# Optimization experiments

Measured on AMD Instinct MI355X. Metric: run time of the kernel, lower is better.

## Reference

```python
import jax, jax.numpy as jnp
import numpy as np

EMB = 128
EA = 32
ET = 32
N = 50000
E = 500000
EPS = 1e-5
DROP_P = 0.1


def setup_inputs() -> dict:
    key = jax.random.key(0)
    ks = jax.random.split(key, 12)
    din = EMB + EA + ET
    return {
        "hidden": jax.random.normal(ks[0], (N, EMB), jnp.float32),
        "edge_index": jax.random.randint(ks[1], (2, E), 0, N, jnp.int64 if jax.config.jax_enable_x64 else jnp.int32),
        "edge_attr": jax.random.normal(ks[2], (E, EA), jnp.float32),
        "edge_time_emb": jax.random.normal(ks[3], (E, ET), jnp.float32),
        "boundary_condition": jax.random.normal(ks[4], (N, EMB), jnp.float32),
        # learned params (torch Linear stored transposed: [in, out])
        "W_msg": jax.random.normal(ks[5], (din, EMB), jnp.float32) / np.sqrt(din),
        "b_msg": jnp.zeros((EMB,), jnp.float32),
        "W_lin": jax.random.normal(ks[6], (EMB, EMB), jnp.float32) / np.sqrt(EMB),
        "b_lin": jnp.zeros((EMB,), jnp.float32),
        "ln_gamma": jnp.ones((EMB,), jnp.float32),
        "ln_beta": jnp.zeros((EMB,), jnp.float32),
    }


def reference(hidden, edge_index, edge_attr, edge_time_emb, boundary_condition,
              W_msg, b_msg, W_lin, b_lin, ln_gamma, ln_beta):
    num_nodes = hidden.shape[0]
    # gather source node features, concat with edge features -> [E, emb+ea+et]
    msg = jnp.concatenate([hidden[edge_index[0]], edge_attr, edge_time_emb], axis=1)
    msg = jax.nn.relu(msg @ W_msg + b_msg)                      # [E, emb]
    # append boundary condition as self-loop messages
    msg_aug = jnp.concatenate([msg, boundary_condition], axis=0)
    idx_aug = jnp.concatenate([edge_index[1], jnp.arange(num_nodes, dtype=edge_index.dtype)])
    out = jax.ops.segment_sum(msg_aug, idx_aug, num_segments=num_nodes)  # scatter-sum [N, emb]
    out = out @ W_lin + b_lin
    # LayerNorm (eps=1e-5, affine)
    mean = out.mean(-1, keepdims=True)
    var = out.var(-1, keepdims=True)
    out = (out - mean) * jax.lax.rsqrt(var + EPS) * ln_gamma + ln_beta
    out = jax.nn.relu(out)
    # dropout p=0.1, training=True (fixed key for reproducibility)
    keep = jax.random.bernoulli(jax.random.key(42), 1.0 - DROP_P, out.shape)
    out = jnp.where(keep, out / (1.0 - DROP_P), 0.0)
    return out
```

## Files before the change

### kernel.cpp

```cpp
#include <hip/hip_runtime.h>
#include <stdint.h>

#define NN 50000
#define NE 500000
#define NEPAD 500032
#define SPB 64
#define HP_BLOCKS ((NN + 127) / 128)
#define DEG_STRIDE (HP_BLOCKS * 256)
#define NBLK_N ((NN + 255) / 256)

typedef short bf16x8 __attribute__((ext_vector_type(8)));
typedef float f32x4 __attribute__((ext_vector_type(4)));
typedef unsigned short u16;
typedef unsigned short u16x4 __attribute__((ext_vector_type(4)));
typedef unsigned int u32x4 __attribute__((ext_vector_type(4)));

__device__ __forceinline__ u16 f2b(float x) {
  uint32_t u = __builtin_bit_cast(uint32_t, x);
  return (u16)((u + 0x7fffu + ((u >> 16) & 1u)) >> 16);
}
__device__ __forceinline__ float b2f(uint32_t lo16) {
  return __builtin_bit_cast(float, lo16 << 16);
}

__device__ __forceinline__ void threefry(uint32_t x0, uint32_t x1,
                                         uint32_t& o0, uint32_t& o1) {
  const uint32_t k0 = 0u, k1 = 42u, k2 = 0u ^ 42u ^ 0x1BD11BDAu;
  x0 += k0; x1 += k1;
#define TFR(r) { x0 += x1; x1 = (x1 << r) | (x1 >> (32 - r)); x1 ^= x0; }
  TFR(13) TFR(15) TFR(26) TFR(6)
  x0 += k1; x1 += k2 + 1u;
  TFR(17) TFR(29) TFR(16) TFR(24)
  x0 += k2; x1 += k0 + 2u;
  TFR(13) TFR(15) TFR(26) TFR(6)
  x0 += k0; x1 += k1 + 3u;
  TFR(17) TFR(29) TFR(16) TFR(24)
  x0 += k1; x1 += k2 + 4u;
  TFR(13) TFR(15) TFR(26) TFR(6)
  x0 += k2; x1 += k0 + 5u;
#undef TFR
  o0 = x0; o1 = x1;
}

__device__ __forceinline__ bool jax_keep(uint32_t j) {
  uint32_t o0, o1;
  threefry(0u, j, o0, o1);
  uint32_t bits = o0 ^ o1;
  float u = __builtin_bit_cast(float, (bits >> 9) | 0x3f800000u) - 1.0f;
  return u < 0.9f;
}

template <int K, int GM>
__device__ __forceinline__ void mfma_tile(const u16* sA, const u16* sBT,
                                          int t, f32x4 (&c)[4][4]) {
  const int lane = t & 63, w = t >> 6;
  const int wr = (w & 1) << 6, wc = (w >> 1) << 6;
  const int quad = lane >> 4, lr = lane & 15;
#pragma unroll
  for (int i = 0; i < 4; ++i)
#pragma unroll
    for (int j = 0; j < 4; ++j) { f32x4 z = {0.f, 0.f, 0.f, 0.f}; c[i][j] = z; }
#pragma unroll
  for (int ks = 0; ks < K; ks += 32) {
    const int kg = (ks >> 3) + quad;
    bf16x8 a[4], b[4];
#pragma unroll
    for (int i = 0; i < 4; ++i) {
      int row = wr + (i << 4) + lr;
      a[i] = *(const bf16x8*)&sA[row * K + ((kg ^ (row & GM)) << 3)];
    }
#pragma unroll
    for (int j = 0; j < 4; ++j) {
      int row = wc + (j << 4) + lr;
      b[j] = *(const bf16x8*)&sBT[row * K + ((kg ^ (row & GM)) << 3)];
    }
#pragma unroll
    for (int i = 0; i < 4; ++i)
#pragma unroll
      for (int j = 0; j < 4; ++j)
        c[i][j] = __builtin_amdgcn_mfma_f32_16x16x32_bf16(a[i], b[j], c[i][j], 0, 0, 0);
  }
}

__global__ __launch_bounds__(256) void k_scan1(const uint32_t* __restrict__ deg,
                                               uint32_t* __restrict__ ex,
                                               uint32_t* __restrict__ bsum) {
  __shared__ uint32_t s[256];
  int t = threadIdx.x;
  int i = blockIdx.x * 256 + t;
  uint32_t v = (i < NN) ? deg[i] : 0u;
  s[t] = v;
  __syncthreads();
#pragma unroll
  for (int off = 1; off < 256; off <<= 1) {
    uint32_t y = (t >= off) ? s[t - off] : 0u;
    __syncthreads();
    s[t] += y;
    __syncthreads();
  }
  if (i < NN) ex[i] = s[t] - v;
  if (t == 255) bsum[blockIdx.x] = s[255];
}

__global__ __launch_bounds__(256) void k_scan2(const uint32_t* __restrict__ bsum,
                                               uint32_t* __restrict__ boff) {
  __shared__ uint32_t s[256];
  int t = threadIdx.x;
  uint32_t v = (t < NBLK_N) ? bsum[t] : 0u;
  s[t] = v;
  __syncthreads();
#pragma unroll
  for (int off = 1; off < 256; off <<= 1) {
    uint32_t y = (t >= off) ? s[t - off] : 0u;
    __syncthreads();
    s[t] += y;
    __syncthreads();
  }
  boff[t] = s[t] - v;
}

__global__ __launch_bounds__(256) void k_scan3(const uint32_t* __restrict__ ex,
                                               const uint32_t* __restrict__ boff,
                                               uint32_t* __restrict__ cursor) {
  int i = blockIdx.x * 256 + threadIdx.x;
  if (i < NN) cursor[i] = ex[i] + boff[blockIdx.x];
}

__global__ __launch_bounds__(256) void k_perm_s(const int* __restrict__ ei,
                                                const float* __restrict__ attr,
                                                const float* __restrict__ tim,
                                                uint32_t* __restrict__ cursor,
                                                u16* __restrict__ Asorted,
                                                int* __restrict__ srcp,
                                                int* __restrict__ dstp) {
  const int t = threadIdx.x;
  const int j = t & 7;
  const long e = (long)blockIdx.x * 32 + (t >> 3);
  const bool v = e < NE;
  int src = 0, dst = 0;
  uint32_t pos = 0;
  if (v && j == 0) {
    src = ei[e];
    dst = ei[NE + e];
    pos = atomicAdd(&cursor[dst], 1u);
  }
  pos = __shfl(pos, 0, 8);
  src = __shfl(src, 0, 8);
  dst = __shfl(dst, 0, 8);
  if (v) {
    f32x4 va = *(const f32x4*)(attr + ((size_t)e << 5) + (j << 2));
    f32x4 vt = *(const f32x4*)(tim + ((size_t)e << 5) + (j << 2));
    u16x4 ba = {f2b(va[0]), f2b(va[1]), f2b(va[2]), f2b(va[3])};
    u16x4 bt = {f2b(vt[0]), f2b(vt[1]), f2b(vt[2]), f2b(vt[3])};
    *(u16x4*)&Asorted[((size_t)pos << 6) + (j << 2)] = ba;
    *(u16x4*)&Asorted[((size_t)pos << 6) + 32 + (j << 2)] = bt;
    if (j == 0) { srcp[pos] = src; dstp[pos] = dst; }
  }
}

__global__ __launch_bounds__(256) void k_perm_f(const int* __restrict__ ei,
                                                uint32_t* __restrict__ cursor,
                                                int* __restrict__ perm,
                                                int* __restrict__ srcp,
                                                int* __restrict__ dstp) {
  int i = blockIdx.x * 256 + threadIdx.x;
  if (i < NE) {
    int s = ei[i], d = ei[NE + i];
    uint32_t pos = atomicAdd(&cursor[d], 1u);
    perm[pos] = i;
    srcp[pos] = s;
    dstp[pos] = d;
  }
}

__global__ __launch_bounds__(256) void k_hp(const float* __restrict__ hidden,
                                            const float* __restrict__ Wmsg,
                                            const float* __restrict__ bmsg,
                                            const int* __restrict__ ei,
                                            uint32_t* __restrict__ deg,
                                            u16* __restrict__ Hp,
                                            u16* __restrict__ WcImg) {
  __shared__ u16 sA[128 * 128];
  __shared__ u16 sBT[128 * 128];
  const int t = threadIdx.x;
  const int row0 = blockIdx.x << 7;
  for (int i = blockIdx.x * 256 + t; i < NE; i += DEG_STRIDE)
    atomicAdd(&deg[ei[NE + i]], 1u);
  if (blockIdx.x == 0) {
#pragma unroll
    for (int it = 0; it < 32; ++it) {
      int li = t + (it << 8);
      int k = li >> 7, d = li & 127;
      WcImg[(d << 6) + k] = f2b(Wmsg[16384 + li]);
    }
  }
#pragma unroll
  for (int it = 0; it < 16; ++it) {
    int li = t + (it << 8);
    int row = li >> 5, c4 = li & 31;
    int n = row0 + row;
    f32x4 v = {0.f, 0.f, 0.f, 0.f};
    if (n < NN) v = *(const f32x4*)(hidden + ((size_t)n << 7) + (c4 << 2));
    u16x4 b = {f2b(v[0]), f2b(v[1]), f2b(v[2]), f2b(v[3])};
    *(u16x4*)&sA[(row << 7) + ((((c4 >> 1) ^ (row & 15)) << 3) + ((c4 & 1) << 2))] = b;
  }
#pragma unroll
  for (int it = 0; it < 64; ++it) {
    int li = t + (it << 8);
    int k = li >> 7, d = li & 127;
    sBT[(d << 7) + ((((k >> 3) ^ (d & 15)) << 3) + (k & 7))] = f2b(Wmsg[li]);
  }
  __syncthreads();
  f32x4 c[4][4];
  mfma_tile<128, 15>(sA, sBT, t, c);
  const int lane = t & 63, w = t >> 6;
  const int wr = (w & 1) << 6, wc = (w >> 1) << 6;
  const int quad = lane >> 4, lr = lane & 15;
#pragma unroll
  for (int j = 0; j < 4; ++j) {
    int d = wc + (j << 4) + lr;
    float bias = bmsg[d];
#pragma unroll
    for (int i = 0; i < 4; ++i) {
      int nb = row0 + wr + (i << 4) + (quad << 2);
#pragma unroll
      for (int r = 0; r < 4; ++r) {
        int n = nb + r;
        if (n < NN) Hp[((size_t)n << 7) + d] = f2b(c[i][j][r] + bias);
      }
    }
  }
}

template <bool SORTED>
__global__ __launch_bounds__(256, 4) void k_edge3(const float* __restrict__ attr,
                                                  const float* __restrict__ tim,
                                                  const int* __restrict__ perm,
                                                  const u16* __restrict__ Asorted,
                                                  const u16* __restrict__ WcImg,
                                                  const int* __restrict__ srcp,
                                                  const int* __restrict__ dstp,
                                                  const u16* __restrict__ Hp,
                                                  float* __restrict__ acc) {
  __shared__ union { u16 A[64 * 64]; float C[64 * 128]; } lds;
  __shared__ int sdst[64];
  const int t = threadIdx.x;
  const long e0 = (long)blockIdx.x << 6;

  if (!SORTED) {
#pragma unroll
    for (int it = 0; it < 2; ++it) {
      int li = t + (it << 8);
      int row = li >> 3, c4 = li & 7;
      long sg = e0 + row;
      f32x4 va = {0.f, 0.f, 0.f, 0.f}, vt = {0.f, 0.f, 0.f, 0.f};
      if (sg < NE) {
        int e = perm[sg];
        va = *(const f32x4*)(attr + ((size_t)e << 5) + (c4 << 2));
        vt = *(const f32x4*)(tim + ((size_t)e << 5) + (c4 << 2));
      }
      int g0 = c4 >> 1, h = (c4 & 1) << 2;
      u16x4 ba = {f2b(va[0]), f2b(va[1]), f2b(va[2]), f2b(va[3])};
      u16x4 bt = {f2b(vt[0]), f2b(vt[1]), f2b(vt[2]), f2b(vt[3])};
      *(u16x4*)&lds.A[(row << 6) + (((g0 ^ (row & 7)) << 3) + h)] = ba;
      *(u16x4*)&lds.A[(row << 6) + ((((g0 + 4) ^ (row & 7)) << 3) + h)] = bt;
    }
  }
  const int s = t >> 2, q = t & 3;
  const long sg1 = e0 + s;
  const bool v1 = sg1 < NE;
  int src = 0, dstn = -1;
  if (v1) { src = srcp[sg1]; dstn = dstp[sg1]; }
  u32x4 hp[4];
  if (v1) {
    const u32x4* hp4 = (const u32x4*)(Hp + ((size_t)src << 7) + (q << 5));
#pragma unroll
    for (int g = 0; g < 4; ++g) hp[g] = hp4[g];
  }
  if (q == 0) sdst[s] = v1 ? dstn : -1;
  __syncthreads();

  const int lane = t & 63, w = t >> 6;
  const int quad = lane >> 4, lr = lane & 15;
  f32x4 c[4][2];
#pragma unroll
  for (int i = 0; i < 4; ++i)
#pragma unroll
    for (int j = 0; j < 2; ++j) { f32x4 z = {0.f, 0.f, 0.f, 0.f}; c[i][j] = z; }
#pragma unroll
  for (int ks = 0; ks < 64; ks += 32) {
    const int gi = (ks >> 3) + quad;
    bf16x8 a[4], b[2];
#pragma unroll
    for (int i = 0; i < 4; ++i) {
      int row = (i << 4) + lr;
      if (SORTED)
        a[i] = *(const bf16x8*)&Asorted[((size_t)(e0 + row) << 6) + (gi << 3)];
      else
        a[i] = *(const bf16x8*)&lds.A[(row << 6) + ((gi ^ (row & 7)) << 3)];
    }
#pragma unroll
    for (int j = 0; j < 2; ++j) {
      int col = (w << 5) + (j << 4) + lr;
      b[j] = *(const bf16x8*)&WcImg[(col << 6) + (gi << 3)];
    }
#pragma unroll
    for (int i = 0; i < 4; ++i)
#pragma unroll
      for (int j = 0; j < 2; ++j)
        c[i][j] = __builtin_amdgcn_mfma_f32_16x16x32_bf16(a[i], b[j], c[i][j], 0, 0, 0);
  }
  __syncthreads();
#pragma unroll
  for (int i = 0; i < 4; ++i)
#pragma unroll
    for (int j = 0; j < 2; ++j)
#pragma unroll
      for (int r = 0; r < 4; ++r) {
        int row = (i << 4) + (quad << 2) + r;
        int col = (w << 5) + (j << 4) + lr;
        lds.C[(row << 7) + ((((col >> 2) ^ (row & 31)) << 2) + (col & 3))] = c[i][j][r];
      }
  __syncthreads();
  if (v1) {
#pragma unroll
    for (int g = 0; g < 8; ++g) {
      int cb = (q << 5) + (g << 2);
      float* p = &lds.C[(s << 7) + ((((cb >> 2) ^ (s & 31)) << 2))];
      f32x4 cv = *(const f32x4*)p;
      uint32_t w0 = hp[g >> 1][(g & 1) << 1];
      uint32_t w1 = hp[g >> 1][((g & 1) << 1) + 1];
      cv[0] = fmaxf(cv[0] + b2f(w0 & 0xffffu), 0.f);
      cv[1] = fmaxf(cv[1] + b2f(w0 >> 16), 0.f);
      cv[2] = fmaxf(cv[2] + b2f(w1 & 0xffffu), 0.f);
      cv[3] = fmaxf(cv[3] + b2f(w1 >> 16), 0.f);
      *(f32x4*)p = cv;
    }
  }
  __syncthreads();
  {
    const int col = t & 127, half = t >> 7;
    const int beg = half << 5, end = beg + 32;
    int cur = sdst[beg];
    float sum = 0.f;
    int runstart = beg;
    for (int ss = beg; ss < end; ++ss) {
      int d = sdst[ss];
      if (d != cur) {
        if (cur >= 0) {
          float* p = acc + ((size_t)cur << 7) + col;
          if (runstart == beg) unsafeAtomicAdd(p, sum);
          else *p = sum;
        }
        cur = d; sum = 0.f; runstart = ss;
      }
      sum += lds.C[(ss << 7) + ((((col >> 2) ^ (ss & 31)) << 2) + (col & 3))];
    }
    if (cur >= 0) unsafeAtomicAdd(acc + ((size_t)cur << 7) + col, sum);
  }
}

__global__ __launch_bounds__(256) void k_out(float* accout,
                                             const float* __restrict__ bnd,
                                             const float* __restrict__ Wlin,
                                             const float* __restrict__ blin,
                                             const float* __restrict__ gam,
                                             const float* __restrict__ bet) {
  __shared__ union {
    struct { u16 A[128 * 128]; u16 BT[128 * 128]; } ab;
    float C[128 * 128];
  } lds;
  const int t = threadIdx.x;
  const int row0 = blockIdx.x << 7;
#pragma unroll
  for (int it = 0; it < 16; ++it) {
    int li = t + (it << 8);
    int row = li >> 5, c4 = li & 31;
    int n = row0 + row;
    f32x4 v = {0.f, 0.f, 0.f, 0.f};
    if (n < NN) {
      f32x4 a = *(const f32x4*)(accout + ((size_t)n << 7) + (c4 << 2));
      f32x4 b = *(const f32x4*)(bnd + ((size_t)n << 7) + (c4 << 2));
      v = a + b;
    }
    u16x4 bb = {f2b(v[0]), f2b(v[1]), f2b(v[2]), f2b(v[3])};
    *(u16x4*)&lds.ab.A[(row << 7) + ((((c4 >> 1) ^ (row & 15)) << 3) + ((c4 & 1) << 2))] = bb;
  }
#pragma unroll
  for (int it = 0; it < 64; ++it) {
    int li = t + (it << 8);
    int k = li >> 7, d = li & 127;
    lds.ab.BT[(d << 7) + ((((k >> 3) ^ (d & 15)) << 3) + (k & 7))] = f2b(Wlin[li]);
  }
  __syncthreads();
  f32x4 c[4][4];
  mfma_tile<128, 15>(lds.ab.A, lds.ab.BT, t, c);
  __syncthreads();
  {
    const int lane = t & 63, w = t >> 6;
    const int wr = (w & 1) << 6, wc = (w >> 1) << 6;
    const int quad = lane >> 4, lr = lane & 15;
#pragma unroll
    for (int i = 0; i < 4; ++i)
#pragma unroll
      for (int j = 0; j < 4; ++j)
#pragma unroll
        for (int r = 0; r < 4; ++r) {
          int row = wr + (i << 4) + (quad << 2) + r;
          int col = wc + (j << 4) + lr;
          lds.C[(row << 7) + ((((col >> 2) ^ (row & 31)) << 2) + (col & 3))] = c[i][j][r];
        }
  }
  __syncthreads();
  const int row = t >> 1, off = (t & 1) << 6;
  const int n = row0 + row;
  float s1 = 0.f, s2 = 0.f;
  if (n < NN) {
    for (int g = 0; g < 16; ++g) {
      int cb = off + (g << 2);
      f32x4 cv = *(const f32x4*)&lds.C[(row << 7) + (((cb >> 2) ^ (row & 31)) << 2)];
#pragma unroll
      for (int q = 0; q < 4; ++q) {
        float x = cv[q] + blin[cb + q];
        s1 += x; s2 += x * x;
      }
    }
  }
  s1 += __shfl_xor(s1, 1, 64);
  s2 += __shfl_xor(s2, 1, 64);
  if (n < NN) {
    const float mean = s1 * 0.0078125f;
    const float var = s2 * 0.0078125f - mean * mean;
    const float inv = 1.0f / sqrtf(var + 1e-5f);
    for (int g = 0; g < 16; ++g) {
      int cb = off + (g << 2);
      f32x4 cv = *(const f32x4*)&lds.C[(row << 7) + (((cb >> 2) ^ (row & 31)) << 2)];
#pragma unroll
      for (int q = 0; q < 4; ++q) {
        int d = cb + q;
        float x = cv[q] + blin[d];
        float y = (x - mean) * inv * gam[d] + bet[d];
        y = fmaxf(y, 0.f);
        uint32_t jj = ((uint32_t)n << 7) + (uint32_t)d;
        accout[((size_t)n << 7) + d] = jax_keep(jj) ? (y * (1.0f / 0.9f)) : 0.0f;
      }
    }
  }
}

extern "C" void kernel_launch(void* const* d_in, const int* in_sizes, int n_in,
                              void* d_out, int out_size, void* d_ws, size_t ws_size,
                              hipStream_t stream) {
  (void)in_sizes; (void)n_in; (void)out_size;
  const float* hidden = (const float*)d_in[0];
  const int*   ei     = (const int*)d_in[1];
  const float* attr   = (const float*)d_in[2];
  const float* tim    = (const float*)d_in[3];
  const float* bnd    = (const float*)d_in[4];
  const float* Wmsg   = (const float*)d_in[5];
  const float* bmsg   = (const float*)d_in[6];
  const float* Wlin   = (const float*)d_in[7];
  const float* blin   = (const float*)d_in[8];
  const float* gam    = (const float*)d_in[9];
  const float* bet    = (const float*)d_in[10];

  float* acc = (float*)d_out;

  char* ws = (char*)d_ws;
  u16*      Hp     = (u16*)(ws + 0);
  u16*      WcImg  = (u16*)(ws + 12800000);
  uint32_t* deg    = (uint32_t*)(ws + 12816384);
  uint32_t* cursor = (uint32_t*)(ws + 13016384);
  uint32_t* bsum   = (uint32_t*)(ws + 13216384);
  uint32_t* boff   = (uint32_t*)(ws + 13217408);
  uint32_t* ex     = (uint32_t*)(ws + 13218432);
  int*      srcp   = (int*)(ws + 13418432);
  int*      dstp   = (int*)(ws + 15418432);
  u16*      Asort  = (u16*)(ws + 17418432);
  int*      perm   = (int*)(ws + 17418432);
  const bool sorted = ws_size >= (size_t)(17418432 + (size_t)NEPAD * 64 * 2);

  hipMemsetAsync(deg, 0, (size_t)NN * 4, stream);
  hipMemsetAsync(acc, 0, (size_t)NN * 128 * 4, stream);

  k_hp   <<<dim3(HP_BLOCKS), dim3(256), 0, stream>>>(hidden, Wmsg, bmsg, ei, deg, Hp, WcImg);
  k_scan1<<<dim3(NBLK_N), dim3(256), 0, stream>>>(deg, ex, bsum);
  k_scan2<<<dim3(1), dim3(256), 0, stream>>>(bsum, boff);
  k_scan3<<<dim3(NBLK_N), dim3(256), 0, stream>>>(ex, boff, cursor);
  if (sorted) {
    k_perm_s<<<dim3((NE + 31) / 32), dim3(256), 0, stream>>>(ei, attr, tim, cursor, Asort, srcp, dstp);
    k_edge3<true><<<dim3(NEPAD / SPB), dim3(256), 0, stream>>>(attr, tim, nullptr, Asort, WcImg, srcp, dstp, Hp, acc);
  } else {
    k_perm_f<<<dim3((NE + 255) / 256), dim3(256), 0, stream>>>(ei, cursor, perm, srcp, dstp);
    k_edge3<false><<<dim3(NEPAD / SPB), dim3(256), 0, stream>>>(attr, tim, perm, nullptr, WcImg, srcp, dstp, Hp, acc);
  }
  k_out  <<<dim3((NN + 127) / 128), dim3(256), 0, stream>>>(acc, bnd, Wlin, blin, gam, bet);
}
```

Before: 387.7 us.

## Pre-convert weights once, shrink node GEMM tiles, pack src/dst indices

Adds a small prep kernel that converts W_msg and W_lin to transposed bf16 images once, so the node-level GEMM kernels no longer rebuild a 128x128 weight tile in LDS per block and instead read B fragments straight from global/L2. The node kernels (k_hp, k_out) shrink from 128-row to 64-row tiles, which cuts LDS use and doubles block count for occupancy. Edge src/dst indices are packed into one 32-bit word (16 bits each), halving index traffic. k_out's LayerNorm/dropout epilogue is vectorised with float4 loads and stores. Packing assumes node ids fit in 16 bits, but N=50000 fits.

After: 369.8 us. 4.6% less time.

```diff
diff --git a/kernel.cpp b/kernel.cpp
--- a/kernel.cpp
+++ b/kernel.cpp
@@ -5,8 +5,8 @@
 #define NE 500000
 #define NEPAD 500032
 #define SPB 64
-#define HP_BLOCKS ((NN + 127) / 128)
-#define DEG_STRIDE (HP_BLOCKS * 256)
+#define NT_BLOCKS ((NN + 63) / 64)
+#define DEG_STRIDE (NT_BLOCKS * 256)
 #define NBLK_N ((NN + 255) / 256)
 
 typedef short bf16x8 __attribute__((ext_vector_type(8)));
@@ -50,35 +50,39 @@
   return u < 0.9f;
 }
 
-template <int K, int GM>
-__device__ __forceinline__ void mfma_tile(const u16* sA, const u16* sBT,
-                                          int t, f32x4 (&c)[4][4]) {
-  const int lane = t & 63, w = t >> 6;
-  const int wr = (w & 1) << 6, wc = (w >> 1) << 6;
-  const int quad = lane >> 4, lr = lane & 15;
-#pragma unroll
-  for (int i = 0; i < 4; ++i)
-#pragma unroll
-    for (int j = 0; j < 4; ++j) { f32x4 z = {0.f, 0.f, 0.f, 0.f}; c[i][j] = z; }
-#pragma unroll
-  for (int ks = 0; ks < K; ks += 32) {
-    const int kg = (ks >> 3) + quad;
-    bf16x8 a[4], b[4];
-#pragma unroll
-    for (int i = 0; i < 4; ++i) {
-      int row = wr + (i << 4) + lr;
-      a[i] = *(const bf16x8*)&sA[row * K + ((kg ^ (row & GM)) << 3)];
-    }
-#pragma unroll
-    for (int j = 0; j < 4; ++j) {
-      int row = wc + (j << 4) + lr;
-      b[j] = *(const bf16x8*)&sBT[row * K + ((kg ^ (row & GM)) << 3)];
-    }
-#pragma unroll
-    for (int i = 0; i < 4; ++i)
-#pragma unroll
-      for (int j = 0; j < 4; ++j)
-        c[i][j] = __builtin_amdgcn_mfma_f32_16x16x32_bf16(a[i], b[j], c[i][j], 0, 0, 0);
+__global__ __launch_bounds__(256) void k_prep(const float* __restrict__ Wmsg,
+                                              const float* __restrict__ Wlin,
+                                              u16* __restrict__ WhImg,
+                                              u16* __restrict__ WcImg,
+                                              u16* __restrict__ WlImg) {
+  const int t = threadIdx.x, b = blockIdx.x;
+  if (b == 0) {
+#pragma unroll
+    for (int it = 0; it < 16; ++it) {
+      int g = t + (it << 8);
+      int d = g >> 5, k4 = (g & 31) << 2;
+      u16x4 v = {f2b(Wmsg[(k4 + 0) * 128 + d]), f2b(Wmsg[(k4 + 1) * 128 + d]),
+                 f2b(Wmsg[(k4 + 2) * 128 + d]), f2b(Wmsg[(k4 + 3) * 128 + d])};
+      *(u16x4*)&WhImg[(d << 7) + k4] = v;
+    }
+  } else if (b == 1) {
+#pragma unroll
+    for (int it = 0; it < 8; ++it) {
+      int g = t + (it << 8);
+      int d = g >> 4, k4 = (g & 15) << 2;
+      u16x4 v = {f2b(Wmsg[(128 + k4 + 0) * 128 + d]), f2b(Wmsg[(128 + k4 + 1) * 128 + d]),
+                 f2b(Wmsg[(128 + k4 + 2) * 128 + d]), f2b(Wmsg[(128 + k4 + 3) * 128 + d])};
+      *(u16x4*)&WcImg[(d << 6) + k4] = v;
+    }
+  } else {
+#pragma unroll
+    for (int it = 0; it < 16; ++it) {
+      int g = t + (it << 8);
+      int d = g >> 5, k4 = (g & 31) << 2;
+      u16x4 v = {f2b(Wlin[(k4 + 0) * 128 + d]), f2b(Wlin[(k4 + 1) * 128 + d]),
+                 f2b(Wlin[(k4 + 2) * 128 + d]), f2b(Wlin[(k4 + 3) * 128 + d])};
+      *(u16x4*)&WlImg[(d << 7) + k4] = v;
+    }
   }
 }
 
@@ -131,22 +135,19 @@
                                                 const float* __restrict__ tim,
                                                 uint32_t* __restrict__ cursor,
                                                 u16* __restrict__ Asorted,
-                                                int* __restrict__ srcp,
-                                                int* __restrict__ dstp) {
+                                                uint32_t* __restrict__ sd) {
   const int t = threadIdx.x;
   const int j = t & 7;
   const long e = (long)blockIdx.x * 32 + (t >> 3);
   const bool v = e < NE;
-  int src = 0, dst = 0;
-  uint32_t pos = 0;
+  uint32_t pos = 0, sdv = 0;
   if (v && j == 0) {
-    src = ei[e];
-    dst = ei[NE + e];
+    uint32_t src = (uint32_t)ei[e];
+    uint32_t dst = (uint32_t)ei[NE + e];
+    sdv = src | (dst << 16);
     pos = atomicAdd(&cursor[dst], 1u);
   }
   pos = __shfl(pos, 0, 8);
-  src = __shfl(src, 0, 8);
-  dst = __shfl(dst, 0, 8);
   if (v) {
     f32x4 va = *(const f32x4*)(attr + ((size_t)e << 5) + (j << 2));
     f32x4 vt = *(const f32x4*)(tim + ((size_t)e << 5) + (j << 2));
@@ -154,48 +155,36 @@
     u16x4 bt = {f2b(vt[0]), f2b(vt[1]), f2b(vt[2]), f2b(vt[3])};
     *(u16x4*)&Asorted[((size_t)pos << 6) + (j << 2)] = ba;
     *(u16x4*)&Asorted[((size_t)pos << 6) + 32 + (j << 2)] = bt;
-    if (j == 0) { srcp[pos] = src; dstp[pos] = dst; }
+    if (j == 0) sd[pos] = sdv;
   }
 }
 
 __global__ __launch_bounds__(256) void k_perm_f(const int* __restrict__ ei,
                                                 uint32_t* __restrict__ cursor,
                                                 int* __restrict__ perm,
-                                                int* __restrict__ srcp,
-                                                int* __restrict__ dstp) {
+                                                uint32_t* __restrict__ sd) {
   int i = blockIdx.x * 256 + threadIdx.x;
   if (i < NE) {
-    int s = ei[i], d = ei[NE + i];
+    uint32_t s = (uint32_t)ei[i], d = (uint32_t)ei[NE + i];
     uint32_t pos = atomicAdd(&cursor[d], 1u);
     perm[pos] = i;
-    srcp[pos] = s;
-    dstp[pos] = d;
+    sd[pos] = s | (d << 16);
   }
 }
 
 __global__ __launch_bounds__(256) void k_hp(const float* __restrict__ hidden,
-                                            const float* __restrict__ Wmsg,
+                                            const u16* __restrict__ WhImg,
                                             const float* __restrict__ bmsg,
                                             const int* __restrict__ ei,
                                             uint32_t* __restrict__ deg,
-                                            u16* __restrict__ Hp,
-                                            u16* __restrict__ WcImg) {
-  __shared__ u16 sA[128 * 128];
-  __shared__ u16 sBT[128 * 128];
+                                            u16* __restrict__ Hp) {
+  __shared__ u16 sA[64 * 128];
   const int t = threadIdx.x;
-  const int row0 = blockIdx.x << 7;
+  const int row0 = blockIdx.x << 6;
   for (int i = blockIdx.x * 256 + t; i < NE; i += DEG_STRIDE)
     atomicAdd(&deg[ei[NE + i]], 1u);
-  if (blockIdx.x == 0) {
-#pragma unroll
-    for (int it = 0; it < 32; ++it) {
-      int li = t + (it << 8);
-      int k = li >> 7, d = li & 127;
-      WcImg[(d << 6) + k] = f2b(Wmsg[16384 + li]);
-    }
-  }
-#pragma unroll
-  for (int it = 0; it < 16; ++it) {
+#pragma unroll
+  for (int it = 0; it < 8; ++it) {
     int li = t + (it << 8);
     int row = li >> 5, c4 = li & 31;
     int n = row0 + row;
@@ -204,25 +193,41 @@
     u16x4 b = {f2b(v[0]), f2b(v[1]), f2b(v[2]), f2b(v[3])};
     *(u16x4*)&sA[(row << 7) + ((((c4 >> 1) ^ (row & 15)) << 3) + ((c4 & 1) << 2))] = b;
   }
-#pragma unroll
-  for (int it = 0; it < 64; ++it) {
-    int li = t + (it << 8);
-    int k = li >> 7, d = li & 127;
-    sBT[(d << 7) + ((((k >> 3) ^ (d & 15)) << 3) + (k & 7))] = f2b(Wmsg[li]);
-  }
-  __syncthreads();
-  f32x4 c[4][4];
-  mfma_tile<128, 15>(sA, sBT, t, c);
+  __syncthreads();
   const int lane = t & 63, w = t >> 6;
-  const int wr = (w & 1) << 6, wc = (w >> 1) << 6;
   const int quad = lane >> 4, lr = lane & 15;
-#pragma unroll
-  for (int j = 0; j < 4; ++j) {
-    int d = wc + (j << 4) + lr;
+  f32x4 c[4][2];
+#pragma unroll
+  for (int i = 0; i < 4; ++i)
+#pragma unroll
+    for (int j = 0; j < 2; ++j) { f32x4 z = {0.f, 0.f, 0.f, 0.f}; c[i][j] = z; }
+#pragma unroll
+  for (int ks = 0; ks < 128; ks += 32) {
+    const int gi = (ks >> 3) + quad;
+    bf16x8 a[4], b[2];
+#pragma unroll
+    for (int i = 0; i < 4; ++i) {
+      int row = (i << 4) + lr;
+      a[i] = *(const bf16x8*)&sA[(row << 7) + ((gi ^ (row & 15)) << 3)];
+    }
+#pragma unroll
+    for (int j = 0; j < 2; ++j) {
+      int col = (w << 5) + (j << 4) + lr;
+      b[j] = *(const bf16x8*)&WhImg[(col << 7) + (gi << 3)];
+    }
+#pragma unroll
+    for (int i = 0; i < 4; ++i)
+#pragma unroll
+      for (int j = 0; j < 2; ++j)
+        c[i][j] = __builtin_amdgcn_mfma_f32_16x16x32_bf16(a[i], b[j], c[i][j], 0, 0, 0);
+  }
+#pragma unroll
+  for (int j = 0; j < 2; ++j) {
+    int d = (w << 5) + (j << 4) + lr;
     float bias = bmsg[d];
 #pragma unroll
     for (int i = 0; i < 4; ++i) {
-      int nb = row0 + wr + (i << 4) + (quad << 2);
+      int nb = row0 + (i << 4) + (quad << 2);
 #pragma unroll
       for (int r = 0; r < 4; ++r) {
         int n = nb + r;
@@ -238,8 +243,7 @@
                                                   const int* __restrict__ perm,
                                                   const u16* __restrict__ Asorted,
                                                   const u16* __restrict__ WcImg,
-                                                  const int* __restrict__ srcp,
-                                                  const int* __restrict__ dstp,
+                                                  const uint32_t* __restrict__ sd,
                                                   const u16* __restrict__ Hp,
                                                   float* __restrict__ acc) {
   __shared__ union { u16 A[64 * 64]; float C[64 * 128]; } lds;
@@ -270,7 +274,11 @@
   const long sg1 = e0 + s;
   const bool v1 = sg1 < NE;
   int src = 0, dstn = -1;
-  if (v1) { src = srcp[sg1]; dstn = dstp[sg1]; }
+  if (v1) {
+    uint32_t sdv = sd[sg1];
+    src = (int)(sdv & 0xffffu);
+    dstn = (int)(sdv >> 16);
+  }
   u32x4 hp[4];
   if (v1) {
     const u32x4* hp4 = (const u32x4*)(Hp + ((size_t)src << 7) + (q << 5));
@@ -362,18 +370,15 @@
 
 __global__ __launch_bounds__(256) void k_out(float* accout,
                                              const float* __restrict__ bnd,
-                                             const float* __restrict__ Wlin,
+                                             const u16* __restrict__ WlImg,
                                              const float* __restrict__ blin,
                                              const float* __restrict__ gam,
                                              const float* __restrict__ bet) {
-  __shared__ union {
-    struct { u16 A[128 * 128]; u16 BT[128 * 128]; } ab;
-    float C[128 * 128];
-  } lds;
+  __shared__ union { u16 A[64 * 128]; float C[64 * 128]; } lds;
   const int t = threadIdx.x;
-  const int row0 = blockIdx.x << 7;
-#pragma unroll
-  for (int it = 0; it < 16; ++it) {
+  const int row0 = blockIdx.x << 6;
+#pragma unroll
+  for (int it = 0; it < 8; ++it) {
     int li = t + (it << 8);
     int row = li >> 5, c4 = li & 31;
     int n = row0 + row;
@@ -384,66 +389,87 @@
       v = a + b;
     }
     u16x4 bb = {f2b(v[0]), f2b(v[1]), f2b(v[2]), f2b(v[3])};
-    *(u16x4*)&lds.ab.A[(row << 7) + ((((c4 >> 1) ^ (row & 15)) << 3) + ((c4 & 1) << 2))] = bb;
-  }
-#pragma unroll
-  for (int it = 0; it < 64; ++it) {
-    int li = t + (it << 8);
-    int k = li >> 7, d = li & 127;
-    lds.ab.BT[(d << 7) + ((((k >> 3) ^ (d & 15)) << 3) + (k & 7))] = f2b(Wlin[li]);
-  }
-  __syncthreads();
-  f32x4 c[4][4];
-  mfma_tile<128, 15>(lds.ab.A, lds.ab.BT, t, c);
-  __syncthreads();
-  {
-    const int lane = t & 63, w = t >> 6;
-    const int wr = (w & 1) << 6, wc = (w >> 1) << 6;
-    const int quad = lane >> 4, lr = lane & 15;
+    *(u16x4*)&lds.A[(row << 7) + ((((c4 >> 1) ^ (row & 15)) << 3) + ((c4 & 1) << 2))] = bb;
+  }
+  __syncthreads();
+  const int lane = t & 63, w = t >> 6;
+  const int quad = lane >> 4, lr = lane & 15;
+  f32x4 c[4][2];
+#pragma unroll
+  for (int i = 0; i < 4; ++i)
+#pragma unroll
+    for (int j = 0; j < 2; ++j) { f32x4 z = {0.f, 0.f, 0.f, 0.f}; c[i][j] = z; }
+#pragma unroll
+  for (int ks = 0; ks < 128; ks += 32) {
+    const int gi = (ks >> 3) + quad;
+    bf16x8 a[4], b[2];
+#pragma unroll
+    for (int i = 0; i < 4; ++i) {
+      int row = (i << 4) + lr;
+      a[i] = *(const bf16x8*)&lds.A[(row << 7) + ((gi ^ (row & 15)) << 3)];
+    }
+#pragma unroll
+    for (int j = 0; j < 2; ++j) {
+      int col = (w << 5) + (j << 4) + lr;
+      b[j] = *(const bf16x8*)&WlImg[(col << 7) + (gi << 3)];
+    }
 #pragma unroll
     for (int i = 0; i < 4; ++i)
 #pragma unroll
-      for (int j = 0; j < 4; ++j)
-#pragma unroll
-        for (int r = 0; r < 4; ++r) {
-          int row = wr + (i << 4) + (quad << 2) + r;
-          int col = wc + (j << 4) + lr;
-          lds.C[(row << 7) + ((((col >> 2) ^ (row & 31)) << 2) + (col & 3))] = c[i][j][r];
-        }
-  }
-  __syncthreads();
-  const int row = t >> 1, off = (t & 1) << 6;
+      for (int j = 0; j < 2; ++j)
+        c[i][j] = __builtin_amdgcn_mfma_f32_16x16x32_bf16(a[i], b[j], c[i][j], 0, 0, 0);
+  }
+  __syncthreads();
+#pragma unroll
+  for (int i = 0; i < 4; ++i)
+#pragma unroll
+    for (int j = 0; j < 2; ++j)
+#pragma unroll
+      for (int r = 0; r < 4; ++r) {
+        int row = (i << 4) + (quad << 2) + r;
+        int col = (w << 5) + (j << 4) + lr;
+        lds.C[(row << 7) + ((((col >> 2) ^ (row & 31)) << 2) + (col & 3))] = c[i][j][r];
+      }
+  __syncthreads();
+  const int row = t >> 2, q = t & 3;
   const int n = row0 + row;
   float s1 = 0.f, s2 = 0.f;
   if (n < NN) {
-    for (int g = 0; g < 16; ++g) {
-      int cb = off + (g << 2);
-      f32x4 cv = *(const f32x4*)&lds.C[(row << 7) + (((cb >> 2) ^ (row & 31)) << 2)];
-#pragma unroll
-      for (int q = 0; q < 4; ++q) {
-        float x = cv[q] + blin[cb + q];
+#pragma unroll
+    for (int g = 0; g < 8; ++g) {
+      int g5 = (q << 3) + g;
+      f32x4 cv = *(const f32x4*)&lds.C[(row << 7) + ((g5 ^ (row & 31)) << 2)];
+      f32x4 bl = *(const f32x4*)(blin + (g5 << 2));
+#pragma unroll
+      for (int m = 0; m < 4; ++m) {
+        float x = cv[m] + bl[m];
         s1 += x; s2 += x * x;
       }
     }
   }
-  s1 += __shfl_xor(s1, 1, 64);
-  s2 += __shfl_xor(s2, 1, 64);
+  s1 += __shfl_xor(s1, 1, 64); s1 += __shfl_xor(s1, 2, 64);
+  s2 += __shfl_xor(s2, 1, 64); s2 += __shfl_xor(s2, 2, 64);
   if (n < NN) {
     const float mean = s1 * 0.0078125f;
     const float var = s2 * 0.0078125f - mean * mean;
     const float inv = 1.0f / sqrtf(var + 1e-5f);
-    for (int g = 0; g < 16; ++g) {
-      int cb = off + (g << 2);
-      f32x4 cv = *(const f32x4*)&lds.C[(row << 7) + (((cb >> 2) ^ (row & 31)) << 2)];
-#pragma unroll
-      for (int q = 0; q < 4; ++q) {
-        int d = cb + q;
-        float x = cv[q] + blin[d];
-        float y = (x - mean) * inv * gam[d] + bet[d];
-        y = fmaxf(y, 0.f);
-        uint32_t jj = ((uint32_t)n << 7) + (uint32_t)d;
-        accout[((size_t)n << 7) + d] = jax_keep(jj) ? (y * (1.0f / 0.9f)) : 0.0f;
-      }
+#pragma unroll
+    for (int g = 0; g < 8; ++g) {
+      int g5 = (q << 3) + g;
+      int d0 = g5 << 2;
+      f32x4 cv = *(const f32x4*)&lds.C[(row << 7) + ((g5 ^ (row & 31)) << 2)];
+      f32x4 bl = *(const f32x4*)(blin + d0);
+      f32x4 gm = *(const f32x4*)(gam + d0);
+      f32x4 bb = *(const f32x4*)(bet + d0);
+      f32x4 o;
+#pragma unroll
+      for (int m = 0; m < 4; ++m) {
+        float x = cv[m] + bl[m];
+        float y = fmaxf((x - mean) * inv * gm[m] + bb[m], 0.f);
+        uint32_t jj = ((uint32_t)n << 7) + (uint32_t)(d0 + m);
+        o[m] = jax_keep(jj) ? (y * (1.0f / 0.9f)) : 0.0f;
+      }
+      *(f32x4*)(accout + ((size_t)n << 7) + d0) = o;
     }
   }
 }
@@ -468,31 +494,33 @@
 
   char* ws = (char*)d_ws;
   u16*      Hp     = (u16*)(ws + 0);
-  u16*      WcImg  = (u16*)(ws + 12800000);
-  uint32_t* deg    = (uint32_t*)(ws + 12816384);
-  uint32_t* cursor = (uint32_t*)(ws + 13016384);
-  uint32_t* bsum   = (uint32_t*)(ws + 13216384);
-  uint32_t* boff   = (uint32_t*)(ws + 13217408);
-  uint32_t* ex     = (uint32_t*)(ws + 13218432);
-  int*      srcp   = (int*)(ws + 13418432);
-  int*      dstp   = (int*)(ws + 15418432);
-  u16*      Asort  = (u16*)(ws + 17418432);
-  int*      perm   = (int*)(ws + 17418432);
-  const bool sorted = ws_size >= (size_t)(17418432 + (size_t)NEPAD * 64 * 2);
+  u16*      WhImg  = (u16*)(ws + 12800000);
+  u16*      WcImg  = (u16*)(ws + 12832768);
+  u16*      WlImg  = (u16*)(ws + 12849152);
+  uint32_t* deg    = (uint32_t*)(ws + 12881920);
+  uint32_t* cursor = (uint32_t*)(ws + 13081920);
+  uint32_t* bsum   = (uint32_t*)(ws + 13281920);
+  uint32_t* boff   = (uint32_t*)(ws + 13282944);
+  uint32_t* ex     = (uint32_t*)(ws + 13283968);
+  uint32_t* sd     = (uint32_t*)(ws + 13483968);
+  u16*      Asort  = (u16*)(ws + 15484096);
+  int*      perm   = (int*)(ws + 15484096);
+  const bool sorted = ws_size >= (size_t)(15484096 + (size_t)NEPAD * 64 * 2);
 
   hipMemsetAsync(deg, 0, (size_t)NN * 4, stream);
   hipMemsetAsync(acc, 0, (size_t)NN * 128 * 4, stream);
 
-  k_hp   <<<dim3(HP_BLOCKS), dim3(256), 0, stream>>>(hidden, Wmsg, bmsg, ei, deg, Hp, WcImg);
+  k_prep <<<dim3(3), dim3(256), 0, stream>>>(Wmsg, Wlin, WhImg, WcImg, WlImg);
+  k_hp   <<<dim3(NT_BLOCKS), dim3(256), 0, stream>>>(hidden, WhImg, bmsg, ei, deg, Hp);
   k_scan1<<<dim3(NBLK_N), dim3(256), 0, stream>>>(deg, ex, bsum);
   k_scan2<<<dim3(1), dim3(256), 0, stream>>>(bsum, boff);
   k_scan3<<<dim3(NBLK_N), dim3(256), 0, stream>>>(ex, boff, cursor);
   if (sorted) {
-    k_perm_s<<<dim3((NE + 31) / 32), dim3(256), 0, stream>>>(ei, attr, tim, cursor, Asort, srcp, dstp);
-    k_edge3<true><<<dim3(NEPAD / SPB), dim3(256), 0, stream>>>(attr, tim, nullptr, Asort, WcImg, srcp, dstp, Hp, acc);
+    k_perm_s<<<dim3((NE + 31) / 32), dim3(256), 0, stream>>>(ei, attr, tim, cursor, Asort, sd);
+    k_edge3<true><<<dim3(NEPAD / SPB), dim3(256), 0, stream>>>(attr, tim, nullptr, Asort, WcImg, sd, Hp, acc);
   } else {
-    k_perm_f<<<dim3((NE + 255) / 256), dim3(256), 0, stream>>>(ei, cursor, perm, srcp, dstp);
-    k_edge3<false><<<dim3(NEPAD / SPB), dim3(256), 0, stream>>>(attr, tim, perm, nullptr, WcImg, srcp, dstp, Hp, acc);
-  }
-  k_out  <<<dim3((NN + 127) / 128), dim3(256), 0, stream>>>(acc, bnd, Wlin, blin, gam, bet);
-}
+    k_perm_f<<<dim3((NE + 255) / 256), dim3(256), 0, stream>>>(ei, cursor, perm, sd);
+    k_edge3<false><<<dim3(NEPAD / SPB), dim3(256), 0, stream>>>(attr, tim, perm, nullptr, WcImg, sd, Hp, acc);
+  }
+  k_out  <<<dim3(NT_BLOCKS), dim3(256), 0, stream>>>(acc, bnd, WlImg, blin, gam, bet);
+}
```
